# Kernel optimization log

Hardware: AMD Instinct MI355X
Metric: run time of the kernel (lower is better)

## Reference

```python
import jax, jax.numpy as jnp
import numpy as np

B, S, HID = 2, 2048, 2048
NH, NKV = 16, 4
HD = HID // NH            # 128
N_REP = NH // NKV          # 4
THETA = 10000.0
NEG = -1e9


def _rope_tables(position_ids):
    # inv_freq: [HD/2]
    inv_freq = 1.0 / (THETA ** (jnp.arange(0, HD, 2, dtype=jnp.float32) / HD))
    freqs = position_ids.astype(jnp.float32)[..., None] * inv_freq  # [B,S,HD/2]
    emb = jnp.concatenate([freqs, freqs], axis=-1)                  # [B,S,HD]
    return jnp.cos(emb), jnp.sin(emb)


def _rotate_half(x):
    return jnp.concatenate([-x[..., HD // 2:], x[..., :HD // 2]], axis=-1)


def setup_inputs() -> dict:
    key = jax.random.key(0)
    k1, k2, k3 = jax.random.split(key, 3)
    hidden_states = jax.random.normal(k1, (B, S, HID), dtype=jnp.float32)
    w_qkv = jax.random.normal(k2, (HID + 2 * NKV * HD, HID), dtype=jnp.float32) * 0.02
    w_out = jax.random.normal(k3, (HID, HID), dtype=jnp.float32) * 0.02
    causal = jnp.tril(jnp.ones((S, S), dtype=bool))
    attention_mask = jnp.where(causal, 0.0, NEG).astype(jnp.float32)
    attention_mask = jnp.broadcast_to(attention_mask[None, None], (B, 1, S, S))
    position_ids = jnp.broadcast_to(jnp.arange(S, dtype=jnp.int64), (B, S))
    return {"hidden_states": hidden_states, "w_qkv": w_qkv, "w_out": w_out,
            "attention_mask": attention_mask, "position_ids": position_ids}


def reference(hidden_states, w_qkv, w_out, attention_mask, position_ids):
    bsz, q_len, _ = hidden_states.shape
    qkv = hidden_states @ w_qkv.T                                   # [B,S,HID+2*NKV*HD]
    q, k, v = jnp.split(qkv, [HID, HID + NKV * HD], axis=-1)
    q = q.reshape(bsz, q_len, NH, HD).transpose(0, 2, 1, 3)         # [B,NH,S,HD]
    k = k.reshape(bsz, q_len, NKV, HD).transpose(0, 2, 1, 3)        # [B,NKV,S,HD]
    v = v.reshape(bsz, q_len, NKV, HD).transpose(0, 2, 1, 3)

    cos, sin = _rope_tables(position_ids)                           # [B,S,HD]
    cos, sin = cos[:, None], sin[:, None]                           # unsqueeze head dim
    q = q * cos + _rotate_half(q) * sin
    k = k * cos + _rotate_half(k) * sin

    # GQA: repeat KV heads to match query heads (repeat_kv)
    k = jnp.repeat(k, N_REP, axis=1)                                # [B,NH,S,HD]
    v = jnp.repeat(v, N_REP, axis=1)

    scale = 1.0 / jnp.sqrt(jnp.float32(HD))
    scores = jnp.einsum('bhqd,bhkd->bhqk', q, k) * scale
    scores = scores + attention_mask                                # [B,NH,S,S]
    attn = jax.nn.softmax(scores.astype(jnp.float32), axis=-1).astype(q.dtype)
    out = jnp.einsum('bhqk,bhkd->bhqd', attn, v)                    # [B,NH,S,HD]
    out = out.transpose(0, 2, 1, 3).reshape(bsz, q_len, HID)
    return out @ w_out.T
```

## Files before the change

### kernel.cpp

```cpp
#include <hip/hip_runtime.h>
#include <hip/hip_bf16.h>
#include <math.h>

#define S_LEN   2048
#define HIDDEN  2048
#define NHEADS  16
#define NKVH    4
#define HDIM    128

typedef short  short8  __attribute__((ext_vector_type(8)));
typedef float  floatx4 __attribute__((ext_vector_type(4)));
typedef __hip_bfloat16 bf16;

__device__ inline void async_copy16(const void* g, void* l) {
  __builtin_amdgcn_global_load_lds((__attribute__((address_space(1))) void*)(g),
                                   (__attribute__((address_space(3))) void*)(l),
                                   16, 0, 0);
}

__device__ inline unsigned short cvt1(float x) {
  bf16 t = __float2bfloat16(x);
  return *reinterpret_cast<unsigned short*>(&t);
}
__device__ inline float us2f(unsigned short u) {
  unsigned int v = ((unsigned int)u) << 16;
  return *reinterpret_cast<float*>(&v);
}

#define N8_H  1048576
#define N8_WQ  786432
#define N8_WO  524288
__global__ __launch_bounds__(256) void cvt_all(const float* __restrict__ h,
                                               const float* __restrict__ wq,
                                               const float* __restrict__ wo,
                                               unsigned short* __restrict__ dst) {
  const int i = blockIdx.x * 256 + threadIdx.x;
  if (i >= N8_H + N8_WQ + N8_WO) return;
  const float* src; int j;
  if (i < N8_H)              { src = h;  j = i; }
  else if (i < N8_H + N8_WQ) { src = wq; j = i - N8_H; }
  else                       { src = wo; j = i - N8_H - N8_WQ; }
  const float4 a = reinterpret_cast<const float4*>(src)[j * 2];
  const float4 b = reinterpret_cast<const float4*>(src)[j * 2 + 1];
  unsigned short o[8] = {cvt1(a.x), cvt1(a.y), cvt1(a.z), cvt1(a.w),
                         cvt1(b.x), cvt1(b.y), cvt1(b.z), cvt1(b.w)};
  *reinterpret_cast<short8*>(dst + (size_t)i * 8) = *reinterpret_cast<short8*>(o);
}

template<int MODE>
__global__ __launch_bounds__(256) void gemm_bt(const bf16* __restrict__ A,
                                               const bf16* __restrict__ B,
                                               int M, int N, int K,
                                               bf16* __restrict__ qbuf,
                                               bf16* __restrict__ kbuf,
                                               bf16* __restrict__ vtbuf,
                                               float* __restrict__ Cout)
{
  __shared__ unsigned short As[128 * 32];
  __shared__ unsigned short Bs[128 * 32];
  const int bn   = blockIdx.x;
  const int bm   = blockIdx.y;
  const int t    = threadIdx.x;
  const int w    = t >> 6;
  const int lane = t & 63;
  const int m16  = lane & 15;
  const int quad = lane >> 4;
  const int wm   = (w >> 1) * 64;
  const int wn   = (w & 1) * 64;

  int bcol[4];
#pragma unroll
  for (int ni = 0; ni < 4; ++ni)
    bcol[ni] = (MODE == 0) ? ((w & 1) * 32 + (ni & 1) * 16 + (ni >> 1) * 64)
                           : (wn + ni * 16);

  const floatx4 zf = {0.f, 0.f, 0.f, 0.f};
  floatx4 acc[4][4];
#pragma unroll
  for (int i = 0; i < 4; ++i)
#pragma unroll
    for (int j = 0; j < 4; ++j) acc[i][j] = zf;

  const bf16* gA = A + (size_t)(bm * 128 + (t >> 2)) * K + (t & 3) * 8;
  const bf16* gB = B + (size_t)(bn * 128 + (t >> 2)) * K + (t & 3) * 8;
  unsigned short* lA = &As[w * 512];
  unsigned short* lB = &Bs[w * 512];

  for (int k0 = 0; k0 < K; k0 += 32) {
    __syncthreads();
#pragma unroll
    for (int i = 0; i < 2; ++i) {
      async_copy16(gA + (size_t)(64 * i) * K + k0, lA + i * 2048);
      async_copy16(gB + (size_t)(64 * i) * K + k0, lB + i * 2048);
    }
    __builtin_amdgcn_s_waitcnt(0);
    __syncthreads();
    short8 af[4], bfr[4];
#pragma unroll
    for (int mi = 0; mi < 4; ++mi)
      af[mi] = *reinterpret_cast<const short8*>(&As[(wm + mi * 16 + m16) * 32 + quad * 8]);
#pragma unroll
    for (int ni = 0; ni < 4; ++ni)
      bfr[ni] = *reinterpret_cast<const short8*>(&Bs[(bcol[ni] + m16) * 32 + quad * 8]);
#pragma unroll
    for (int mi = 0; mi < 4; ++mi)
#pragma unroll
      for (int ni = 0; ni < 4; ++ni)
        acc[mi][ni] = __builtin_amdgcn_mfma_f32_16x16x32_bf16(af[mi], bfr[ni], acc[mi][ni], 0, 0, 0);
  }

  if (MODE == 1) {
#pragma unroll
    for (int mi = 0; mi < 4; ++mi)
#pragma unroll
      for (int ni = 0; ni < 4; ++ni) {
        const int row0 = bm * 128 + wm + mi * 16 + quad * 4;
        const int col  = bn * 128 + bcol[ni] + m16;
#pragma unroll
        for (int r = 0; r < 4; ++r)
          Cout[(size_t)(row0 + r) * N + col] = acc[mi][ni][r];
      }
    return;
  }

  const int colbase = bn * 128;
  if (colbase < HIDDEN + NKVH * HDIM) {
    const bool isQ = (colbase < HIDDEN);
    const float post = isQ ? 0.08838834764831845f : 1.0f;
    float invf[2];
#pragma unroll
    for (int p = 0; p < 2; ++p)
      invf[p] = exp2f((float)((w & 1) * 32 + p * 16 + m16) * -0.2076205059f);
#pragma unroll
    for (int mi = 0; mi < 4; ++mi) {
      const int row0 = bm * 128 + wm + mi * 16 + quad * 4;
#pragma unroll
      for (int r = 0; r < 4; ++r) {
        const int m = row0 + r;
        const int b = m >> 11, s = m & 2047;
        float sn[2], cs[2];
        __sincosf((float)s * invf[0], &sn[0], &cs[0]);
        __sincosf((float)s * invf[1], &sn[1], &cs[1]);
#pragma unroll
        for (int ni = 0; ni < 4; ++ni) {
          const int p = ni & 1;
          const float v  = acc[mi][ni][r];
          const float v2 = acc[mi][ni ^ 2][r];
          const float rot = ((ni < 2) ? (v * cs[p] - v2 * sn[p])
                                      : (v * cs[p] + v2 * sn[p])) * post;
          const int col = colbase + bcol[ni] + m16;
          if (isQ) {
            const int hh = col >> 7, d = col & 127;
            qbuf[(((size_t)(b * NHEADS + hh)) * S_LEN + s) * HDIM + d] = __float2bfloat16(rot);
          } else {
            const int nn = col - HIDDEN; const int hh = nn >> 7, d = nn & 127;
            kbuf[(((size_t)(b * NKVH + hh)) * S_LEN + s) * HDIM + d] = __float2bfloat16(rot);
          }
        }
      }
    }
  } else {
#pragma unroll
    for (int mi = 0; mi < 4; ++mi)
#pragma unroll
      for (int ni = 0; ni < 4; ++ni) {
        const int row0 = bm * 128 + wm + mi * 16 + quad * 4;
        const int col  = colbase + bcol[ni] + m16;
        const int nn = col - HIDDEN - NKVH * HDIM;
        const int hh = nn >> 7, d = nn & 127;
#pragma unroll
        for (int r = 0; r < 4; ++r) {
          const int m = row0 + r;
          const int b = m >> 11, s = m & 2047;
          vtbuf[(((size_t)(b * NKVH + hh)) * HDIM + d) * S_LEN + s] =
              __float2bfloat16(acc[mi][ni][r]);
        }
      }
  }
}

__global__ __launch_bounds__(256) void attn_partial(const bf16* __restrict__ qbuf,
                                                    const bf16* __restrict__ kbuf,
                                                    const bf16* __restrict__ vtbuf,
                                                    unsigned short* __restrict__ pnum,
                                                    float* __restrict__ plsum,
                                                    bf16* __restrict__ abuf)
{
  __shared__ unsigned short Ks[2][4096];
  __shared__ unsigned short Vs[2][4096];
  __shared__ unsigned short Ps[4][1280];
  const int sidx = 110 - blockIdx.x;
  int i2, c, nch;
  if (sidx < 27)      { i2 = sidx;                     c = 0;              nch = 1; }
  else if (sidx < 81) { i2 = 27 + ((sidx - 27) >> 1);  c = (sidx - 27) & 1; nch = 2; }
  else                { i2 = 54 + (sidx - 81) / 3;     c = (sidx - 81) % 3; nch = 3; }
  const int len = i2 + 1;
  const int k0 = (c * len) / nch, k1 = ((c + 1) * len) / nch;
  const int kvh = blockIdx.y, b = blockIdx.z;
  const int t = threadIdx.x, w = t >> 6, lane = t & 63;
  const int m16 = lane & 15, quad = lane >> 4;
  const int h = kvh * 4 + w;

  const bf16* Qp = qbuf + (((size_t)(b * NHEADS + h)) * S_LEN + i2 * 32 + m16) * HDIM;
  short8 qf[2][4];
#pragma unroll
  for (int T = 0; T < 2; ++T)
#pragma unroll
    for (int cc = 0; cc < 4; ++cc)
      qf[T][cc] = *reinterpret_cast<const short8*>(Qp + (size_t)T * 16 * HDIM + cc * 32 + quad * 8);

  const bf16* Kp  = kbuf  + ((size_t)(b * NKVH + kvh)) * S_LEN * HDIM;
  const bf16* Vtp = vtbuf + ((size_t)(b * NKVH + kvh)) * HDIM * S_LEN;

  const int kk = lane >> 4, cK = lane & 15;
  const int rKa = w * 8 + kk, rKb = rKa + 4;
  const int offKa = rKa * 128 + ((cK ^ (rKa & 7)) * 8);
  const int offKb = rKb * 128 + ((cK ^ (rKb & 7)) * 8);
  const int dd = lane >> 2, cV = lane & 3;
  const int dVa = w * 32 + dd, dVb = dVa + 16;
  const int offVa = dVa * 2048 + ((cV ^ ((dVa >> 1) & 3)) * 8);
  const int offVb = dVb * 2048 + ((cV ^ ((dVb >> 1) & 3)) * 8);

  const floatx4 zf = {0.f, 0.f, 0.f, 0.f};
  floatx4 oacc[2][8];
#pragma unroll
  for (int T = 0; T < 2; ++T)
#pragma unroll
    for (int d = 0; d < 8; ++d) oacc[T][d] = zf;
  floatx4 lacc[2] = {zf, zf};
  unsigned short ones_s[8] = {0x3F80,0x3F80,0x3F80,0x3F80,0x3F80,0x3F80,0x3F80,0x3F80};
  const short8 ones = *reinterpret_cast<short8*>(ones_s);

  unsigned short* Pw = &Ps[w][0];

  {
    const int ks = k0 * 32;
    async_copy16(Kp + (size_t)ks * 128 + offKa, &Ks[0][w * 1024]);
    async_copy16(Kp + (size_t)ks * 128 + offKb, &Ks[0][w * 1024 + 512]);
    async_copy16(Vtp + ks + offVa, &Vs[0][w * 1024]);
    async_copy16(Vtp + ks + offVb, &Vs[0][w * 1024 + 512]);
  }
  __syncthreads();

  for (int ki = k0; ki < k1; ++ki) {
    const int buf = (ki - k0) & 1;
    if (ki + 1 < k1) {
      const int ks = (ki + 1) * 32;
      async_copy16(Kp + (size_t)ks * 128 + offKa, &Ks[buf ^ 1][w * 1024]);
      async_copy16(Kp + (size_t)ks * 128 + offKb, &Ks[buf ^ 1][w * 1024 + 512]);
      async_copy16(Vtp + ks + offVa, &Vs[buf ^ 1][w * 1024]);
      async_copy16(Vtp + ks + offVb, &Vs[buf ^ 1][w * 1024 + 512]);
    }
    const int ks = ki * 32;
    floatx4 s00 = zf, s01 = zf, s10 = zf, s11 = zf;
#pragma unroll
    for (int cc = 0; cc < 4; ++cc) {
      const int sw = ((cc * 4 + quad) ^ (m16 & 7)) * 8;
      short8 kf0 = *reinterpret_cast<const short8*>(&Ks[buf][m16 * 128 + sw]);
      short8 kf1 = *reinterpret_cast<const short8*>(&Ks[buf][(16 + m16) * 128 + sw]);
      s00 = __builtin_amdgcn_mfma_f32_16x16x32_bf16(qf[0][cc], kf0, s00, 0, 0, 0);
      s01 = __builtin_amdgcn_mfma_f32_16x16x32_bf16(qf[0][cc], kf1, s01, 0, 0, 0);
      s10 = __builtin_amdgcn_mfma_f32_16x16x32_bf16(qf[1][cc], kf0, s10, 0, 0, 0);
      s11 = __builtin_amdgcn_mfma_f32_16x16x32_bf16(qf[1][cc], kf1, s11, 0, 0, 0);
    }
#pragma unroll
    for (int T = 0; T < 2; ++T) {
      const floatx4& sa = T ? s10 : s00;
      const floatx4& sb = T ? s11 : s01;
#pragma unroll
      for (int r = 0; r < 4; ++r) {
        const int row = i2 * 32 + T * 16 + quad * 4 + r;
        const float p0 = (ks + m16      > row) ? 0.f : __expf(sa[r]);
        const float p1 = (ks + 16 + m16 > row) ? 0.f : __expf(sb[r]);
        Pw[(T * 16 + quad * 4 + r) * 40 + m16]      = cvt1(p0);
        Pw[(T * 16 + quad * 4 + r) * 40 + 16 + m16] = cvt1(p1);
      }
    }
    const short8 pa0 = *reinterpret_cast<const short8*>(&Pw[m16 * 40 + quad * 8]);
    const short8 pa1 = *reinterpret_cast<const short8*>(&Pw[(16 + m16) * 40 + quad * 8]);
    lacc[0] = __builtin_amdgcn_mfma_f32_16x16x32_bf16(pa0, ones, lacc[0], 0, 0, 0);
    lacc[1] = __builtin_amdgcn_mfma_f32_16x16x32_bf16(pa1, ones, lacc[1], 0, 0, 0);
#pragma unroll
    for (int dt = 0; dt < 8; ++dt) {
      short8 vfr = *reinterpret_cast<const short8*>(
          &Vs[buf][(dt * 16 + m16) * 32 + ((quad ^ ((m16 >> 1) & 3)) * 8)]);
      oacc[0][dt] = __builtin_amdgcn_mfma_f32_16x16x32_bf16(pa0, vfr, oacc[0][dt], 0, 0, 0);
      oacc[1][dt] = __builtin_amdgcn_mfma_f32_16x16x32_bf16(pa1, vfr, oacc[1][dt], 0, 0, 0);
    }
    __syncthreads();
  }

  if (nch == 1) {
#pragma unroll
    for (int T = 0; T < 2; ++T) {
      float invl[4];
#pragma unroll
      for (int r = 0; r < 4; ++r) invl[r] = 1.0f / lacc[T][r];
      bf16* op = abuf + (((size_t)b * S_LEN + i2 * 32 + T * 16 + quad * 4) * NHEADS + h) * HDIM + m16;
#pragma unroll
      for (int dt = 0; dt < 8; ++dt)
#pragma unroll
        for (int r = 0; r < 4; ++r)
          op[(size_t)r * NHEADS * HDIM + dt * 16] = __float2bfloat16(oacc[T][dt][r] * invl[r]);
    }
  } else {
    const int b0 = (i2 < 54) ? (27 + 2 * (i2 - 27)) : (81 + 3 * (i2 - 54));
    const int slot = (b * NHEADS + h) * 111 + b0 + c;
    unsigned short* np = pnum + (size_t)slot * 4096;
#pragma unroll
    for (int T = 0; T < 2; ++T)
#pragma unroll
      for (int dt = 0; dt < 8; ++dt)
#pragma unroll
        for (int r = 0; r < 4; ++r)
          np[(T * 16 + quad * 4 + r) * 128 + dt * 16 + m16] = cvt1(oacc[T][dt][r]);
    if (m16 == 0) {
#pragma unroll
      for (int T = 0; T < 2; ++T)
#pragma unroll
        for (int r = 0; r < 4; ++r)
          plsum[slot * 32 + T * 16 + quad * 4 + r] = lacc[T][r];
    }
  }
}

__global__ __launch_bounds__(256) void attn_combine(const unsigned short* __restrict__ pnum,
                                                    const float* __restrict__ plsum,
                                                    bf16* __restrict__ abuf)
{
  const int i = 54 + blockIdx.x;
  const int h = blockIdx.y, b = blockIdx.z;
  const int i2 = i >> 1, lr0 = (i & 1) * 16;
  const int t = threadIdx.x, row16 = t >> 4, c0 = (t & 15) * 8;
  const int lr = lr0 + row16;
  const int nch = (i2 < 54) ? 2 : 3;
  const int b0  = (i2 < 54) ? (27 + 2 * (i2 - 27)) : (81 + 3 * (i2 - 54));
  const int hb = (b * NHEADS + h) * 111 + b0;
  float acc[8] = {0.f,0.f,0.f,0.f,0.f,0.f,0.f,0.f};
  float lsum = 0.f;
  for (int c = 0; c < nch; ++c) {
    const unsigned short* np = pnum + (size_t)(hb + c) * 4096 + lr * 128 + c0;
    const short8 v = *reinterpret_cast<const short8*>(np);
#pragma unroll
    for (int j = 0; j < 8; ++j) acc[j] += us2f(((unsigned short*)&v)[j]);
    lsum += plsum[(hb + c) * 32 + lr];
  }
  const float invl = 1.0f / lsum;
  unsigned short o[8];
#pragma unroll
  for (int j = 0; j < 8; ++j) o[j] = cvt1(acc[j] * invl);
  *reinterpret_cast<short8*>(abuf + (((size_t)b * S_LEN + i * 16 + row16) * NHEADS + h) * HDIM + c0)
      = *reinterpret_cast<short8*>(o);
}

extern "C" void kernel_launch(void* const* d_in, const int* in_sizes, int n_in,
                              void* d_out, int out_size, void* d_ws, size_t ws_size,
                              hipStream_t stream) {
  const float* hidden_f = (const float*)d_in[0];
  const float* wqkv_f   = (const float*)d_in[1];
  const float* wout_f   = (const float*)d_in[2];
  float* out = (float*)d_out;

  char* ws = (char*)d_ws;
  bf16* hbf    = (bf16*)(ws);
  bf16* wqkvbf = (bf16*)(ws + 16777216);
  bf16* woutbf = (bf16*)(ws + 29360128);
  bf16* qbuf   = (bf16*)(ws + 37748736);
  bf16* kbuf   = (bf16*)(ws + 54525952);
  bf16* vtbuf  = (bf16*)(ws + 58720256);
  bf16* abuf   = (bf16*)(ws + 62914560);
  unsigned short* pnum = (unsigned short*)(ws);
  float* plsum = (float*)(ws + 79691776);

  cvt_all<<<9216, 256, 0, stream>>>(hidden_f, wqkv_f, wout_f, (unsigned short*)ws);

  gemm_bt<0><<<dim3(24, 32), 256, 0, stream>>>(hbf, wqkvbf, 4096, 3072, 2048,
                                               qbuf, kbuf, vtbuf, nullptr);
  attn_partial<<<dim3(111, 4, 2), 256, 0, stream>>>(qbuf, kbuf, vtbuf, pnum, plsum, abuf);
  attn_combine<<<dim3(74, 16, 2), 256, 0, stream>>>(pnum, plsum, abuf);
  gemm_bt<1><<<dim3(16, 32), 256, 0, stream>>>(abuf, woutbf, 4096, 2048, 2048,
                                               nullptr, nullptr, nullptr, out);
}
```

Measured before the change: 347.5 us.

## Rewrite GEMMs with larger tiles, 4-slot async LDS pipeline and swizzled layout

Replaces both projection GEMMs with an 8-wave kernel that uses larger tiles (256x256 for QKV, 128x256 for output) and a 4-deep ring of LDS slots. Global-to-LDS loads for the next steps are issued while MFMAs run, with a partial vmcnt wait replacing the full wait and double barrier per step. LDS rows use an XOR swizzle to cut bank conflicts, and MFMA sections get raised wave priority. The larger tiles mean fewer blocks (192 and 256), which may underfill the GPU's compute units, and the loop keeps prefetching wrapped-around steps past the end, doing redundant loads.

```diff
diff --git a/kernel.cpp b/kernel.cpp
--- a/kernel.cpp
+++ b/kernel.cpp
@@ -48,134 +48,179 @@
 }
 
 template<int MODE>
-__global__ __launch_bounds__(256) void gemm_bt(const bf16* __restrict__ A,
-                                               const bf16* __restrict__ B,
-                                               int M, int N, int K,
-                                               bf16* __restrict__ qbuf,
-                                               bf16* __restrict__ kbuf,
-                                               bf16* __restrict__ vtbuf,
-                                               float* __restrict__ Cout)
+__global__ __launch_bounds__(512, 2) void gemm8(const bf16* __restrict__ A,
+                                                const bf16* __restrict__ B,
+                                                bf16* __restrict__ qbuf,
+                                                bf16* __restrict__ kbuf,
+                                                bf16* __restrict__ vtbuf,
+                                                float* __restrict__ Cout)
 {
-  __shared__ unsigned short As[128 * 32];
-  __shared__ unsigned short Bs[128 * 32];
-  const int bn   = blockIdx.x;
-  const int bm   = blockIdx.y;
-  const int t    = threadIdx.x;
-  const int w    = t >> 6;
-  const int lane = t & 63;
-  const int m16  = lane & 15;
-  const int quad = lane >> 4;
-  const int wm   = (w >> 1) * 64;
-  const int wn   = (w & 1) * 64;
+  constexpr int K      = 2048;
+  constexpr int BM     = (MODE == 0) ? 256 : 128;
+  constexpr int BN     = 256;
+  constexpr int MF     = BM / 32;
+  constexpr int AI     = BM / 128;
+  constexpr int ABYTES = BM * 64;
+  constexpr int SLOT   = (BM + BN) * 64;
+  constexpr int NSTEP  = K / 32;
+
+  __shared__ __align__(16) unsigned short smem[SLOT * 4 / 2];
+  char* smb = (char*)smem;
+
+  const int bn = blockIdx.x, bm = blockIdx.y;
+  const int t = threadIdx.x, w = t >> 6, lane = t & 63;
+  const int m16 = lane & 15, quad = lane >> 4;
+  const int wmr = (w >> 2) * (BM / 2);
+  const int wn  = w & 3;
 
   int bcol[4];
 #pragma unroll
   for (int ni = 0; ni < 4; ++ni)
-    bcol[ni] = (MODE == 0) ? ((w & 1) * 32 + (ni & 1) * 16 + (ni >> 1) * 64)
-                           : (wn + ni * 16);
+    bcol[ni] = (MODE == 0)
+             ? ((wn >> 1) * 128 + (wn & 1) * 32 + (ni & 1) * 16 + (ni >> 1) * 64)
+             : (wn * 64 + ni * 16);
+
+  int afo[MF], bfo[4];
+#pragma unroll
+  for (int mf = 0; mf < MF; ++mf) {
+    const int r = wmr + mf * 16 + m16;
+    afo[mf] = r * 64 + ((quad ^ ((r >> 1) & 3)) << 4);
+  }
+#pragma unroll
+  for (int ni = 0; ni < 4; ++ni) {
+    const int r = bcol[ni] + m16;
+    bfo[ni] = ABYTES + r * 64 + ((quad ^ ((r >> 1) & 3)) << 4);
+  }
+
+  const bf16* srcA[AI]; int dstA[AI];
+#pragma unroll
+  for (int j = 0; j < AI; ++j) {
+    const int ci  = w * AI + j;
+    const int row = ci * 16 + (lane >> 2);
+    const int sl  = (lane & 3) ^ ((row >> 1) & 3);
+    srcA[j] = A + (size_t)(bm * BM + row) * K + sl * 8;
+    dstA[j] = ci * 1024;
+  }
+  const bf16* srcB[2]; int dstB[2];
+#pragma unroll
+  for (int j = 0; j < 2; ++j) {
+    const int ci  = w * 2 + j;
+    const int row = ci * 16 + (lane >> 2);
+    const int sl  = (lane & 3) ^ ((row >> 1) & 3);
+    srcB[j] = B + (size_t)(bn * BN + row) * K + sl * 8;
+    dstB[j] = ABYTES + ci * 1024;
+  }
+
+  auto stage = [&](int step, int slotbyte) {
+#pragma unroll
+    for (int j = 0; j < AI; ++j)
+      async_copy16(srcA[j] + step * 32, smb + slotbyte + dstA[j]);
+#pragma unroll
+    for (int j = 0; j < 2; ++j)
+      async_copy16(srcB[j] + step * 32, smb + slotbyte + dstB[j]);
+  };
 
   const floatx4 zf = {0.f, 0.f, 0.f, 0.f};
-  floatx4 acc[4][4];
-#pragma unroll
-  for (int i = 0; i < 4; ++i)
-#pragma unroll
-    for (int j = 0; j < 4; ++j) acc[i][j] = zf;
-
-  const bf16* gA = A + (size_t)(bm * 128 + (t >> 2)) * K + (t & 3) * 8;
-  const bf16* gB = B + (size_t)(bn * 128 + (t >> 2)) * K + (t & 3) * 8;
-  unsigned short* lA = &As[w * 512];
-  unsigned short* lB = &Bs[w * 512];
-
-  for (int k0 = 0; k0 < K; k0 += 32) {
-    __syncthreads();
-#pragma unroll
-    for (int i = 0; i < 2; ++i) {
-      async_copy16(gA + (size_t)(64 * i) * K + k0, lA + i * 2048);
-      async_copy16(gB + (size_t)(64 * i) * K + k0, lB + i * 2048);
-    }
-    __builtin_amdgcn_s_waitcnt(0);
-    __syncthreads();
-    short8 af[4], bfr[4];
-#pragma unroll
-    for (int mi = 0; mi < 4; ++mi)
-      af[mi] = *reinterpret_cast<const short8*>(&As[(wm + mi * 16 + m16) * 32 + quad * 8]);
+  floatx4 acc[MF][4];
+#pragma unroll
+  for (int mf = 0; mf < MF; ++mf)
+#pragma unroll
+    for (int ni = 0; ni < 4; ++ni) acc[mf][ni] = zf;
+
+  stage(0, 0); stage(1, SLOT); stage(2, 2 * SLOT);
+
+#pragma unroll 4
+  for (int s = 0; s < NSTEP; ++s) {
+    __builtin_amdgcn_sched_barrier(0);
+    if constexpr (MODE == 0) asm volatile("s_waitcnt vmcnt(8)" ::: "memory");
+    else                     asm volatile("s_waitcnt vmcnt(6)" ::: "memory");
+    __builtin_amdgcn_s_barrier();
+    __builtin_amdgcn_sched_barrier(0);
+    const int sb = (s & 3) * SLOT;
+    short8 af[MF], bfr[4];
+#pragma unroll
+    for (int mf = 0; mf < MF; ++mf)
+      af[mf] = *reinterpret_cast<const short8*>(smb + sb + afo[mf]);
 #pragma unroll
     for (int ni = 0; ni < 4; ++ni)
-      bfr[ni] = *reinterpret_cast<const short8*>(&Bs[(bcol[ni] + m16) * 32 + quad * 8]);
-#pragma unroll
-    for (int mi = 0; mi < 4; ++mi)
+      bfr[ni] = *reinterpret_cast<const short8*>(smb + sb + bfo[ni]);
+    stage((s + 3) & (NSTEP - 1), ((s + 3) & 3) * SLOT);
+    __builtin_amdgcn_s_setprio(1);
+#pragma unroll
+    for (int mf = 0; mf < MF; ++mf)
 #pragma unroll
       for (int ni = 0; ni < 4; ++ni)
-        acc[mi][ni] = __builtin_amdgcn_mfma_f32_16x16x32_bf16(af[mi], bfr[ni], acc[mi][ni], 0, 0, 0);
-  }
-
-  if (MODE == 1) {
-#pragma unroll
-    for (int mi = 0; mi < 4; ++mi)
+        acc[mf][ni] = __builtin_amdgcn_mfma_f32_16x16x32_bf16(af[mf], bfr[ni], acc[mf][ni], 0, 0, 0);
+    __builtin_amdgcn_s_setprio(0);
+  }
+  __builtin_amdgcn_s_waitcnt(0);
+
+  if constexpr (MODE == 1) {
+#pragma unroll
+    for (int mf = 0; mf < MF; ++mf)
 #pragma unroll
       for (int ni = 0; ni < 4; ++ni) {
-        const int row0 = bm * 128 + wm + mi * 16 + quad * 4;
-        const int col  = bn * 128 + bcol[ni] + m16;
+        const int row0 = bm * BM + wmr + mf * 16 + quad * 4;
+        const int col  = bn * BN + bcol[ni] + m16;
 #pragma unroll
         for (int r = 0; r < 4; ++r)
-          Cout[(size_t)(row0 + r) * N + col] = acc[mi][ni][r];
+          Cout[(size_t)(row0 + r) * HIDDEN + col] = acc[mf][ni][r];
       }
-    return;
-  }
-
-  const int colbase = bn * 128;
-  if (colbase < HIDDEN + NKVH * HDIM) {
-    const bool isQ = (colbase < HIDDEN);
-    const float post = isQ ? 0.08838834764831845f : 1.0f;
-    float invf[2];
-#pragma unroll
-    for (int p = 0; p < 2; ++p)
-      invf[p] = exp2f((float)((w & 1) * 32 + p * 16 + m16) * -0.2076205059f);
-#pragma unroll
-    for (int mi = 0; mi < 4; ++mi) {
-      const int row0 = bm * 128 + wm + mi * 16 + quad * 4;
-#pragma unroll
-      for (int r = 0; r < 4; ++r) {
-        const int m = row0 + r;
-        const int b = m >> 11, s = m & 2047;
-        float sn[2], cs[2];
-        __sincosf((float)s * invf[0], &sn[0], &cs[0]);
-        __sincosf((float)s * invf[1], &sn[1], &cs[1]);
-#pragma unroll
-        for (int ni = 0; ni < 4; ++ni) {
-          const int p = ni & 1;
-          const float v  = acc[mi][ni][r];
-          const float v2 = acc[mi][ni ^ 2][r];
-          const float rot = ((ni < 2) ? (v * cs[p] - v2 * sn[p])
-                                      : (v * cs[p] + v2 * sn[p])) * post;
-          const int col = colbase + bcol[ni] + m16;
-          if (isQ) {
-            const int hh = col >> 7, d = col & 127;
-            qbuf[(((size_t)(b * NHEADS + hh)) * S_LEN + s) * HDIM + d] = __float2bfloat16(rot);
-          } else {
-            const int nn = col - HIDDEN; const int hh = nn >> 7, d = nn & 127;
-            kbuf[(((size_t)(b * NKVH + hh)) * S_LEN + s) * HDIM + d] = __float2bfloat16(rot);
+  } else {
+    const int colbase = bn * BN;
+    if (colbase < HIDDEN + NKVH * HDIM) {
+      const bool isQ = (colbase < HIDDEN);
+      const float post = isQ ? 0.08838834764831845f : 1.0f;
+      float invf[2];
+#pragma unroll
+      for (int p = 0; p < 2; ++p)
+        invf[p] = exp2f((float)((wn & 1) * 32 + p * 16 + m16) * -0.2076205059f);
+#pragma unroll
+      for (int mf = 0; mf < MF; ++mf) {
+        const int row0 = bm * BM + wmr + mf * 16 + quad * 4;
+#pragma unroll
+        for (int r = 0; r < 4; ++r) {
+          const int m = row0 + r;
+          const int b = m >> 11, s = m & 2047;
+          float sn[2], cs[2];
+          __sincosf((float)s * invf[0], &sn[0], &cs[0]);
+          __sincosf((float)s * invf[1], &sn[1], &cs[1]);
+#pragma unroll
+          for (int ni = 0; ni < 4; ++ni) {
+            const int p = ni & 1;
+            const float v  = acc[mf][ni][r];
+            const float v2 = acc[mf][ni ^ 2][r];
+            const float rot = ((ni < 2) ? (v * cs[p] - v2 * sn[p])
+                                        : (v * cs[p] + v2 * sn[p])) * post;
+            const int col = colbase + bcol[ni] + m16;
+            if (isQ) {
+              const int hh = col >> 7, d = col & 127;
+              qbuf[(((size_t)(b * NHEADS + hh)) * S_LEN + s) * HDIM + d] = __float2bfloat16(rot);
+            } else {
+              const int nn = col - HIDDEN; const int hh = nn >> 7, d = nn & 127;
+              kbuf[(((size_t)(b * NKVH + hh)) * S_LEN + s) * HDIM + d] = __float2bfloat16(rot);
+            }
           }
         }
       }
-    }
-  } else {
-#pragma unroll
-    for (int mi = 0; mi < 4; ++mi)
-#pragma unroll
-      for (int ni = 0; ni < 4; ++ni) {
-        const int row0 = bm * 128 + wm + mi * 16 + quad * 4;
-        const int col  = colbase + bcol[ni] + m16;
-        const int nn = col - HIDDEN - NKVH * HDIM;
-        const int hh = nn >> 7, d = nn & 127;
-#pragma unroll
-        for (int r = 0; r < 4; ++r) {
-          const int m = row0 + r;
-          const int b = m >> 11, s = m & 2047;
-          vtbuf[(((size_t)(b * NKVH + hh)) * HDIM + d) * S_LEN + s] =
-              __float2bfloat16(acc[mi][ni][r]);
+    } else {
+#pragma unroll
+      for (int mf = 0; mf < MF; ++mf)
+#pragma unroll
+        for (int ni = 0; ni < 4; ++ni) {
+          const int col = colbase + bcol[ni] + m16;
+          const int nn = col - HIDDEN - NKVH * HDIM;
+          const int hh = nn >> 7, d = nn & 127;
+          const int row0 = bm * BM + wmr + mf * 16 + quad * 4;
+#pragma unroll
+          for (int r = 0; r < 4; ++r) {
+            const int m = row0 + r;
+            const int b = m >> 11, s = m & 2047;
+            vtbuf[(((size_t)(b * NKVH + hh)) * HDIM + d) * S_LEN + s] =
+                __float2bfloat16(acc[mf][ni][r]);
+          }
         }
-      }
+    }
   }
 }
 
@@ -374,10 +419,8 @@
 
   cvt_all<<<9216, 256, 0, stream>>>(hidden_f, wqkv_f, wout_f, (unsigned short*)ws);
 
-  gemm_bt<0><<<dim3(24, 32), 256, 0, stream>>>(hbf, wqkvbf, 4096, 3072, 2048,
-                                               qbuf, kbuf, vtbuf, nullptr);
+  gemm8<0><<<dim3(12, 16), 512, 0, stream>>>(hbf, wqkvbf, qbuf, kbuf, vtbuf, nullptr);
   attn_partial<<<dim3(111, 4, 2), 256, 0, stream>>>(qbuf, kbuf, vtbuf, pnum, plsum, abuf);
   attn_combine<<<dim3(74, 16, 2), 256, 0, stream>>>(pnum, plsum, abuf);
-  gemm_bt<1><<<dim3(16, 32), 256, 0, stream>>>(abuf, woutbf, 4096, 2048, 2048,
-                                               nullptr, nullptr, nullptr, out);
-}
+  gemm8<1><<<dim3(8, 32), 512, 0, stream>>>(abuf, woutbf, nullptr, nullptr, nullptr, out);
+}
```

Measured after the change: 302.7 us. -12.9%, faster.
